# Performance work log

Measured on AMD Instinct MI355X. Metric: run time of the kernel, lower is better.

Reference implementation:

```python
import jax, jax.numpy as jnp
import numpy as np

DECAY = 0.8
CODEBOOK_SIZE = 1024
DIM = 128


def setup_inputs() -> dict:
    key = jax.random.key(0)
    k1, k2 = jax.random.split(key)
    x = jax.random.normal(k1, (16, 4096, DIM), dtype=jnp.float32)
    embed = jax.random.normal(k2, (CODEBOOK_SIZE, DIM), dtype=jnp.float32)
    ema_embed = embed * 1.0  # ema_num_initial = 1.0
    ema_num = jnp.ones((CODEBOOK_SIZE,), dtype=jnp.float32)
    return {"x": x, "embed": embed, "ema_embed": ema_embed, "ema_num": ema_num}


def reference(x, embed, ema_embed, ema_num):
    # flatten: [..., d] -> [N, d]
    shape = x.shape
    flatten = x.reshape(-1, shape[-1])  # [N, d]
    distance = -2.0 * (flatten @ embed.T) + jnp.sum(embed * embed, axis=-1)  # [N, K]
    embed_ind = jnp.argmin(distance, axis=-1)  # [N]
    quantize = embed[embed_ind.reshape(shape[:-1])]  # gather -> [..., d]

    # training branch: onehot^T @ flatten == segment_sum over code indices
    num_curr = jax.ops.segment_sum(
        jnp.ones_like(embed_ind, dtype=jnp.float32), embed_ind,
        num_segments=CODEBOOK_SIZE)  # [K]
    embed_curr = jax.ops.segment_sum(
        flatten.astype(jnp.float32), embed_ind,
        num_segments=CODEBOOK_SIZE)  # [K, d]

    ema_num_new = ema_num * DECAY + (1.0 - DECAY) * num_curr
    ema_embed_new = ema_embed * DECAY + (1.0 - DECAY) * embed_curr
    embed_new = ema_embed_new / ema_num_new[:, None]
    return quantize, embed_new, ema_embed_new, ema_num_new
```

## Files before the change

kernel.cpp:

```cpp
#include <hip/hip_runtime.h>

#define NPTS   65536
#define DIM    128
#define KCODES 1024
#define BM     128
#define TILE_C 64
#define NTHR   256

typedef short bf16x8 __attribute__((ext_vector_type(8)));
typedef float f32x4  __attribute__((ext_vector_type(4)));

__device__ __forceinline__ short f2bf(float f) {
    unsigned u = __builtin_bit_cast(unsigned, f);
    u = (u + 0x7fffu + ((u >> 16) & 1u)) >> 16;
    return (short)u;
}
__device__ __forceinline__ float bf2f(short s) {
    unsigned u = ((unsigned)(unsigned short)s) << 16;
    return __builtin_bit_cast(float, u);
}
__device__ __forceinline__ void gload_lds16(const void* g, void* l) {
    __builtin_amdgcn_global_load_lds(
        (const __attribute__((address_space(1))) void*)g,
        (__attribute__((address_space(3))) void*)l, 16, 0, 0);
}

__global__ __launch_bounds__(256)
void halfnorm_kernel(const float* __restrict__ embed, float* __restrict__ hn)
{
    const int w    = (blockIdx.x * blockDim.x + threadIdx.x) >> 6;
    const int lane = threadIdx.x & 63;
    if (w < KCODES) {
        float v0 = embed[(long)w * DIM + lane];
        float v1 = embed[(long)w * DIM + 64 + lane];
        float s  = v0 * v0 + v1 * v1;
        #pragma unroll
        for (int off = 32; off > 0; off >>= 1) s += __shfl_xor(s, off);
        if (lane == 0) hn[w] = 0.5f * s;
    }
}

__global__ __launch_bounds__(256)
void pack_kernel(const float* __restrict__ embed, short* __restrict__ ebf,
                 int* __restrict__ ghist, const float* __restrict__ ema_embed,
                 float* __restrict__ acc)
{
    const int g   = blockIdx.x * 256 + threadIdx.x;
    if (g < KCODES) ghist[g] = 0;
    {
        float4 e = reinterpret_cast<const float4*>(ema_embed)[g];
        float4 o = {0.8f * e.x, 0.8f * e.y, 0.8f * e.z, 0.8f * e.w};
        reinterpret_cast<float4*>(acc)[g] = o;
    }
    const int tc  = g >> 11;
    const int f   = (g >> 6) & 31;
    const int l   = g & 63;
    const int h   = f >> 4;
    const int nt  = (f >> 2) & 3;
    const int akk = f & 3;
    const int hg  = l >> 4;
    const int n   = l & 15;
    const int c   = tc * TILE_C + nt * 16 + n;
    const int d0  = akk * 32 + hg * 8;
    const float* src = embed + (long)c * DIM + d0;
    float4 v0 = *reinterpret_cast<const float4*>(src);
    float4 v1 = *reinterpret_cast<const float4*>(src + 4);
    float vv[8] = {v0.x, v0.y, v0.z, v0.w, v1.x, v1.y, v1.z, v1.w};
    bf16x8 out;
    #pragma unroll
    for (int j = 0; j < 8; ++j) {
        short hi = f2bf(vv[j]);
        out[j] = h ? f2bf(vv[j] - bf2f(hi)) : hi;
    }
    *reinterpret_cast<bf16x8*>(ebf + (long)g * 8) = out;
}

__global__ __launch_bounds__(NTHR, 2)
void argmin_kernel(const float* __restrict__ x, const short* __restrict__ ebf,
                   const float* __restrict__ halfnorm, const float* __restrict__ embed,
                   int* __restrict__ ind, float* __restrict__ quant,
                   int* __restrict__ ghist)
{
    __shared__ short es[2][16384];
    __shared__ float hn_lds[KCODES];
    __shared__ int   hist[KCODES];
    __shared__ int   bidx[BM];

    const int t    = threadIdx.x;
    const int lane = t & 63;
    const int w    = t >> 6;
    const int r16  = lane & 15;
    const int h4   = lane >> 4;
    const long xbase = (long)blockIdx.x * BM * DIM;
    const int  wp    = w * 32;

    for (int i = t; i < KCODES; i += NTHR) hist[i] = 0;

    bf16x8 ahi[2][4], alo[2][4];
    #pragma unroll
    for (int ms = 0; ms < 2; ++ms) {
        const long prow = xbase + (long)(wp + ms * 16 + r16) * DIM;
        #pragma unroll
        for (int kk = 0; kk < 4; ++kk) {
            const float* s = x + prow + kk * 32 + h4 * 8;
            float4 u0 = *reinterpret_cast<const float4*>(s);
            float4 u1 = *reinterpret_cast<const float4*>(s + 4);
            float vv[8] = {u0.x, u0.y, u0.z, u0.w, u1.x, u1.y, u1.z, u1.w};
            #pragma unroll
            for (int j = 0; j < 8; ++j) {
                short hi = f2bf(vv[j]);
                ahi[ms][kk][j] = hi;
                alo[ms][kk][j] = f2bf(vv[j] - bf2f(hi));
            }
        }
    }
    reinterpret_cast<float4*>(hn_lds)[t] = reinterpret_cast<const float4*>(halfnorm)[t];

    #pragma unroll
    for (int i = 0; i < 8; ++i) {
        const int f = w * 8 + i;
        gload_lds16(ebf + (long)f * 512 + lane * 8, &es[0][f * 512]);
    }
    __syncthreads();

    float bestv[8];
    int   besti[8];
    #pragma unroll
    for (int s = 0; s < 8; ++s) { bestv[s] = -1e30f; besti[s] = 0; }

    for (int tile = 0; tile < KCODES / TILE_C; ++tile) {
        if (tile + 1 < KCODES / TILE_C) {
            const long gbase = (long)(tile + 1) * 16384;
            #pragma unroll
            for (int i = 0; i < 8; ++i) {
                const int f = w * 8 + i;
                gload_lds16(ebf + gbase + f * 512 + lane * 8, &es[(tile + 1) & 1][f * 512]);
            }
        }

        const short* buf = es[tile & 1];
        f32x4 C[4][2];
        #pragma unroll
        for (int nt = 0; nt < 4; ++nt)
            #pragma unroll
            for (int ms = 0; ms < 2; ++ms) C[nt][ms] = (f32x4){0.f, 0.f, 0.f, 0.f};

        #pragma unroll
        for (int akk = 0; akk < 4; ++akk) {
            #pragma unroll
            for (int nt = 0; nt < 4; ++nt) {
                bf16x8 Bh = *reinterpret_cast<const bf16x8*>(buf + (nt * 4 + akk) * 512 + lane * 8);
                bf16x8 Bl = *reinterpret_cast<const bf16x8*>(buf + (16 + nt * 4 + akk) * 512 + lane * 8);
                C[nt][0] = __builtin_amdgcn_mfma_f32_16x16x32_bf16(ahi[0][akk], Bh, C[nt][0], 0, 0, 0);
                C[nt][1] = __builtin_amdgcn_mfma_f32_16x16x32_bf16(ahi[1][akk], Bh, C[nt][1], 0, 0, 0);
                C[nt][0] = __builtin_amdgcn_mfma_f32_16x16x32_bf16(alo[0][akk], Bh, C[nt][0], 0, 0, 0);
                C[nt][1] = __builtin_amdgcn_mfma_f32_16x16x32_bf16(alo[1][akk], Bh, C[nt][1], 0, 0, 0);
                C[nt][0] = __builtin_amdgcn_mfma_f32_16x16x32_bf16(ahi[0][akk], Bl, C[nt][0], 0, 0, 0);
                C[nt][1] = __builtin_amdgcn_mfma_f32_16x16x32_bf16(ahi[1][akk], Bl, C[nt][1], 0, 0, 0);
            }
        }

        #pragma unroll
        for (int nt = 0; nt < 4; ++nt) {
            const int   c   = tile * TILE_C + nt * 16 + r16;
            const float hnv = hn_lds[c];
            #pragma unroll
            for (int ms = 0; ms < 2; ++ms)
                #pragma unroll
                for (int reg = 0; reg < 4; ++reg) {
                    float sc  = C[nt][ms][reg] - hnv;
                    int  slot = ms * 4 + reg;
                    if (sc > bestv[slot]) { bestv[slot] = sc; besti[slot] = c; }
                }
        }
        __syncthreads();
    }

    #pragma unroll
    for (int s = 0; s < 8; ++s) {
        float v = bestv[s];
        int   i = besti[s];
        #pragma unroll
        for (int off = 1; off < 16; off <<= 1) {
            float ov = __shfl_xor(v, off);
            int   oi = __shfl_xor(i, off);
            if (ov > v || (ov == v && oi < i)) { v = ov; i = oi; }
        }
        bestv[s] = v; besti[s] = i;
    }
    if (r16 == 0) {
        #pragma unroll
        for (int s = 0; s < 8; ++s) {
            int ms = s >> 2, reg = s & 3;
            int p  = wp + ms * 16 + h4 * 4 + reg;
            bidx[p] = besti[s];
            ind[blockIdx.x * BM + p] = besti[s];
        }
    }
    __syncthreads();

    if (t < BM) atomicAdd(&hist[bidx[t]], 1);

    float4* dst = reinterpret_cast<float4*>(quant + xbase);
    #pragma unroll
    for (int i = 0; i < 16; ++i) {
        int idx = i * NTHR + t;
        int p   = idx >> 5;
        int q   = idx & 31;
        int c   = bidx[p];
        dst[idx] = reinterpret_cast<const float4*>(embed + (long)c * DIM)[q];
    }

    __syncthreads();
    for (int i = t; i < KCODES; i += NTHR)
        if (hist[i]) atomicAdd(&ghist[i], hist[i]);
}

__global__ __launch_bounds__(1024)
void scan_kernel(const int* __restrict__ ghist, const float* __restrict__ ema_num,
                 float* __restrict__ ema_num_new, int* __restrict__ cursor)
{
    __shared__ int tmp[KCODES];
    const int t = threadIdx.x;
    const int v = ghist[t];
    ema_num_new[t] = ema_num[t] * 0.8f + 0.2f * (float)v;
    tmp[t] = v;
    __syncthreads();
    #pragma unroll
    for (int off = 1; off < KCODES; off <<= 1) {
        int u = (t >= off) ? tmp[t - off] : 0;
        __syncthreads();
        tmp[t] += u;
        __syncthreads();
    }
    cursor[t] = tmp[t] - v;
}

__global__ __launch_bounds__(256)
void scatter_kernel(const int* __restrict__ ind, int* __restrict__ cursor,
                    int* __restrict__ sorted, int* __restrict__ scode)
{
    const int p = blockIdx.x * 256 + threadIdx.x;
    const int c = ind[p];
    const int pos = atomicAdd(&cursor[c], 1);
    sorted[pos] = p;
    scode[pos]  = c;
}

__global__ __launch_bounds__(128)
void sum2_kernel(const float* __restrict__ x, const int* __restrict__ sorted,
                 const int* __restrict__ scode, float* __restrict__ acc)
{
    __shared__ int sp[64];
    __shared__ int sc[64];
    const int t = threadIdx.x;
    const int base = blockIdx.x * 64;
    if (t < 64) { sp[t] = sorted[base + t]; sc[t] = scode[base + t]; }
    __syncthreads();

    float a = 0.f;
    int cprev = sc[0];
    #pragma unroll 1
    for (int kk = 0; kk < 8; ++kk) {
        float v[8];
        #pragma unroll
        for (int i = 0; i < 8; ++i)
            v[i] = x[(long)sp[kk * 8 + i] * DIM + t];
        #pragma unroll
        for (int i = 0; i < 8; ++i) {
            const int c = sc[kk * 8 + i];
            if (c != cprev) {
                atomicAdd(&acc[(long)cprev * DIM + t], 0.2f * a);
                a = 0.f; cprev = c;
            }
            a += v[i];
        }
    }
    atomicAdd(&acc[(long)cprev * DIM + t], 0.2f * a);
}

__global__ __launch_bounds__(256)
void final_kernel(const float* __restrict__ acc, const float* __restrict__ ema_num_new,
                  float* __restrict__ embed_new)
{
    const int g = blockIdx.x * 256 + threadIdx.x;
    float4 v = reinterpret_cast<const float4*>(acc)[g];
    const float en = ema_num_new[g >> 5];
    float4 o = {v.x / en, v.y / en, v.z / en, v.w / en};
    reinterpret_cast<float4*>(embed_new)[g] = o;
}

extern "C" void kernel_launch(void* const* d_in, const int* in_sizes, int n_in,
                              void* d_out, int out_size, void* d_ws, size_t ws_size,
                              hipStream_t stream)
{
    const float* x         = (const float*)d_in[0];
    const float* embed     = (const float*)d_in[1];
    const float* ema_embed = (const float*)d_in[2];
    const float* ema_num   = (const float*)d_in[3];

    float* out0 = (float*)d_out;
    float* out1 = out0 + 8388608;
    float* out2 = out1 + 131072;
    float* out3 = out2 + 131072;

    char*  ws     = (char*)d_ws;
    float* hn     = (float*)ws;
    int*   ind    = (int*)(ws + 4096);
    short* ebf    = (short*)(ws + 266240);
    int*   ghist  = (int*)(ws + 790528);
    int*   cursor = (int*)(ws + 794624);
    int*   sorted = (int*)(ws + 798720);
    int*   scode  = (int*)(ws + 1060864);

    halfnorm_kernel<<<256, 256, 0, stream>>>(embed, hn);
    pack_kernel<<<128, 256, 0, stream>>>(embed, ebf, ghist, ema_embed, out2);
    argmin_kernel<<<NPTS / BM, NTHR, 0, stream>>>(x, ebf, hn, embed, ind, out0, ghist);
    scan_kernel<<<1, 1024, 0, stream>>>(ghist, ema_num, out3, cursor);
    scatter_kernel<<<NPTS / 256, 256, 0, stream>>>(ind, cursor, sorted, scode);
    sum2_kernel<<<NPTS / 64, 128, 0, stream>>>(x, sorted, scode, out2);
    final_kernel<<<128, 256, 0, stream>>>(out2, out3, out1);
}
```

Measured before the change: 112.9 us.

## Halve codebook tile, drop LDS halfnorm table, fuse halfnorm into pack kernel

Shrinks the codebook tile from 64 to 32 codes so the double-buffered LDS tile is half the size. The 4KB halfnorm LDS table is removed and the per-code half-norms are instead prefetched into registers one tile ahead from global memory. Launch bounds are raised to 4 blocks per CU to get more occupancy. The separate halfnorm kernel is folded into the pack kernel through a block reduction, saving one launch. The cost is twice as many tile iterations and barriers, and fewer MFMAs per LDS sync.

```diff
diff --git a/kernel.cpp b/kernel.cpp
--- a/kernel.cpp
+++ b/kernel.cpp
@@ -4,7 +4,7 @@
 #define DIM    128
 #define KCODES 1024
 #define BM     128
-#define TILE_C 64
+#define TILE_C 32
 #define NTHR   256
 
 typedef short bf16x8 __attribute__((ext_vector_type(8)));
@@ -26,37 +26,25 @@
 }
 
 __global__ __launch_bounds__(256)
-void halfnorm_kernel(const float* __restrict__ embed, float* __restrict__ hn)
-{
-    const int w    = (blockIdx.x * blockDim.x + threadIdx.x) >> 6;
-    const int lane = threadIdx.x & 63;
-    if (w < KCODES) {
-        float v0 = embed[(long)w * DIM + lane];
-        float v1 = embed[(long)w * DIM + 64 + lane];
-        float s  = v0 * v0 + v1 * v1;
-        #pragma unroll
-        for (int off = 32; off > 0; off >>= 1) s += __shfl_xor(s, off);
-        if (lane == 0) hn[w] = 0.5f * s;
-    }
-}
-
-__global__ __launch_bounds__(256)
 void pack_kernel(const float* __restrict__ embed, short* __restrict__ ebf,
                  int* __restrict__ ghist, const float* __restrict__ ema_embed,
-                 float* __restrict__ acc)
-{
-    const int g   = blockIdx.x * 256 + threadIdx.x;
+                 float* __restrict__ acc, float* __restrict__ hn)
+{
+    __shared__ float partial[256];
+    const int t   = threadIdx.x;
+    const int b   = blockIdx.x;
+    const int g   = b * 256 + t;
     if (g < KCODES) ghist[g] = 0;
     {
         float4 e = reinterpret_cast<const float4*>(ema_embed)[g];
         float4 o = {0.8f * e.x, 0.8f * e.y, 0.8f * e.z, 0.8f * e.w};
         reinterpret_cast<float4*>(acc)[g] = o;
     }
-    const int tc  = g >> 11;
-    const int f   = (g >> 6) & 31;
+    const int tc  = g >> 10;
+    const int f   = (g >> 6) & 15;
     const int l   = g & 63;
-    const int h   = f >> 4;
-    const int nt  = (f >> 2) & 3;
+    const int h   = f >> 3;
+    const int nt  = (f >> 2) & 1;
     const int akk = f & 3;
     const int hg  = l >> 4;
     const int n   = l & 15;
@@ -67,22 +55,34 @@
     float4 v1 = *reinterpret_cast<const float4*>(src + 4);
     float vv[8] = {v0.x, v0.y, v0.z, v0.w, v1.x, v1.y, v1.z, v1.w};
     bf16x8 out;
+    float ss = 0.f;
     #pragma unroll
     for (int j = 0; j < 8; ++j) {
         short hi = f2bf(vv[j]);
         out[j] = h ? f2bf(vv[j] - bf2f(hi)) : hi;
+        ss += vv[j] * vv[j];
     }
     *reinterpret_cast<bf16x8*>(ebf + (long)g * 8) = out;
-}
-
-__global__ __launch_bounds__(NTHR, 2)
+
+    if (h == 0) {
+        partial[t] = ss;
+        __syncthreads();
+        if (t < 16) {
+            float s = 0.f;
+            #pragma unroll
+            for (int k = 0; k < 16; ++k) s += partial[t + k * 16];
+            hn[tc * TILE_C + nt * 16 + t] = 0.5f * s;
+        }
+    }
+}
+
+__global__ __launch_bounds__(NTHR, 4)
 void argmin_kernel(const float* __restrict__ x, const short* __restrict__ ebf,
                    const float* __restrict__ halfnorm, const float* __restrict__ embed,
                    int* __restrict__ ind, float* __restrict__ quant,
                    int* __restrict__ ghist)
 {
-    __shared__ short es[2][16384];
-    __shared__ float hn_lds[KCODES];
+    __shared__ short es[2][8192];
     __shared__ int   hist[KCODES];
     __shared__ int   bidx[BM];
 
@@ -114,13 +114,15 @@
             }
         }
     }
-    reinterpret_cast<float4*>(hn_lds)[t] = reinterpret_cast<const float4*>(halfnorm)[t];
-
-    #pragma unroll
-    for (int i = 0; i < 8; ++i) {
-        const int f = w * 8 + i;
+
+    #pragma unroll
+    for (int i = 0; i < 4; ++i) {
+        const int f = w * 4 + i;
         gload_lds16(ebf + (long)f * 512 + lane * 8, &es[0][f * 512]);
     }
+    float hnv_cur[2];
+    #pragma unroll
+    for (int nt = 0; nt < 2; ++nt) hnv_cur[nt] = halfnorm[nt * 16 + r16];
     __syncthreads();
 
     float bestv[8];
@@ -129,28 +131,32 @@
     for (int s = 0; s < 8; ++s) { bestv[s] = -1e30f; besti[s] = 0; }
 
     for (int tile = 0; tile < KCODES / TILE_C; ++tile) {
+        float hnv_nxt[2] = {0.f, 0.f};
         if (tile + 1 < KCODES / TILE_C) {
-            const long gbase = (long)(tile + 1) * 16384;
-            #pragma unroll
-            for (int i = 0; i < 8; ++i) {
-                const int f = w * 8 + i;
+            const long gbase = (long)(tile + 1) * 8192;
+            #pragma unroll
+            for (int i = 0; i < 4; ++i) {
+                const int f = w * 4 + i;
                 gload_lds16(ebf + gbase + f * 512 + lane * 8, &es[(tile + 1) & 1][f * 512]);
             }
+            #pragma unroll
+            for (int nt = 0; nt < 2; ++nt)
+                hnv_nxt[nt] = halfnorm[(tile + 1) * TILE_C + nt * 16 + r16];
         }
 
         const short* buf = es[tile & 1];
-        f32x4 C[4][2];
-        #pragma unroll
-        for (int nt = 0; nt < 4; ++nt)
+        f32x4 C[2][2];
+        #pragma unroll
+        for (int nt = 0; nt < 2; ++nt)
             #pragma unroll
             for (int ms = 0; ms < 2; ++ms) C[nt][ms] = (f32x4){0.f, 0.f, 0.f, 0.f};
 
         #pragma unroll
         for (int akk = 0; akk < 4; ++akk) {
             #pragma unroll
-            for (int nt = 0; nt < 4; ++nt) {
+            for (int nt = 0; nt < 2; ++nt) {
                 bf16x8 Bh = *reinterpret_cast<const bf16x8*>(buf + (nt * 4 + akk) * 512 + lane * 8);
-                bf16x8 Bl = *reinterpret_cast<const bf16x8*>(buf + (16 + nt * 4 + akk) * 512 + lane * 8);
+                bf16x8 Bl = *reinterpret_cast<const bf16x8*>(buf + (8 + nt * 4 + akk) * 512 + lane * 8);
                 C[nt][0] = __builtin_amdgcn_mfma_f32_16x16x32_bf16(ahi[0][akk], Bh, C[nt][0], 0, 0, 0);
                 C[nt][1] = __builtin_amdgcn_mfma_f32_16x16x32_bf16(ahi[1][akk], Bh, C[nt][1], 0, 0, 0);
                 C[nt][0] = __builtin_amdgcn_mfma_f32_16x16x32_bf16(alo[0][akk], Bh, C[nt][0], 0, 0, 0);
@@ -161,18 +167,19 @@
         }
 
         #pragma unroll
-        for (int nt = 0; nt < 4; ++nt) {
-            const int   c   = tile * TILE_C + nt * 16 + r16;
-            const float hnv = hn_lds[c];
+        for (int nt = 0; nt < 2; ++nt) {
+            const int c = tile * TILE_C + nt * 16 + r16;
             #pragma unroll
             for (int ms = 0; ms < 2; ++ms)
                 #pragma unroll
                 for (int reg = 0; reg < 4; ++reg) {
-                    float sc  = C[nt][ms][reg] - hnv;
+                    float sc  = C[nt][ms][reg] - hnv_cur[nt];
                     int  slot = ms * 4 + reg;
                     if (sc > bestv[slot]) { bestv[slot] = sc; besti[slot] = c; }
                 }
         }
+        hnv_cur[0] = hnv_nxt[0];
+        hnv_cur[1] = hnv_nxt[1];
         __syncthreads();
     }
 
@@ -313,8 +320,7 @@
     int*   sorted = (int*)(ws + 798720);
     int*   scode  = (int*)(ws + 1060864);
 
-    halfnorm_kernel<<<256, 256, 0, stream>>>(embed, hn);
-    pack_kernel<<<128, 256, 0, stream>>>(embed, ebf, ghist, ema_embed, out2);
+    pack_kernel<<<128, 256, 0, stream>>>(embed, ebf, ghist, ema_embed, out2, hn);
     argmin_kernel<<<NPTS / BM, NTHR, 0, stream>>>(x, ebf, hn, embed, ind, out0, ghist);
     scan_kernel<<<1, 1024, 0, stream>>>(ghist, ema_num, out3, cursor);
     scatter_kernel<<<NPTS / 256, 256, 0, stream>>>(ind, cursor, sorted, scode);
```

After: 121.8 us. 1.08x slower.
